# Kernel optimization log

Hardware: AMD Instinct MI355X
Metric: run time of the kernel (lower is better)

Reference implementation:

```python
import jax, jax.numpy as jnp
import numpy as np

N = 50000      # nodes
R = 4          # relations
E = 1600000    # edges per relation
IN = 256       # in_feats
H = 256        # h_feats
C = 16         # num_classes


def setup_inputs() -> dict:
    key = jax.random.key(0)
    ks = jax.random.split(key, 8)
    X = jax.random.normal(ks[0], (N, IN), jnp.float32)
    edge_index = jax.random.randint(ks[1], (R, 2, E), 0, N, dtype=jnp.int32)
    W1 = jax.random.normal(ks[2], (R, IN, H), jnp.float32) * (1.0 / np.sqrt(IN))
    W2 = jax.random.normal(ks[3], (R, H, H), jnp.float32) * (1.0 / np.sqrt(H))
    att_q = jax.random.normal(ks[4], (H,), jnp.float32) * (1.0 / np.sqrt(H))
    tau = jnp.asarray(2.0, jnp.float32)
    W_out = jax.random.normal(ks[5], (H, C), jnp.float32) * (1.0 / np.sqrt(H))
    b_out = jnp.zeros((C,), jnp.float32)
    return {"X": X, "edge_index": edge_index, "W1": W1, "W2": W2,
            "att_q": att_q, "tau": tau, "W_out": W_out, "b_out": b_out}


def _sym_norm_spmm(edge, feat):
    """out = D^{-1/2} A D^{-1/2} @ feat for one relation, edge: [2,E]."""
    row, col = edge[0], edge[1]
    ones = jnp.ones(edge.shape[1], feat.dtype)
    deg_r = jax.ops.segment_sum(ones, row, num_segments=N)
    deg_c = jax.ops.segment_sum(ones, col, num_segments=N)
    dinv_r = jax.lax.rsqrt(jnp.maximum(deg_r, 1.0))
    dinv_c = jax.lax.rsqrt(jnp.maximum(deg_c, 1.0))
    w = dinv_r[row] * dinv_c[col]                      # [E]
    msg = w[:, None] * feat[col]                       # gather + scale
    return jax.ops.segment_sum(msg, row, num_segments=N)  # [N, F]


def _rel_layer(edge_index, feat, W):
    # vmapped over relations: ReLU(A_r feat W_r) -> [R, N, H]
    def one(edge, Wr):
        return jax.nn.relu(_sym_norm_spmm(edge, feat) @ Wr)
    return jax.vmap(one)(edge_index, W)


def reference(X, edge_index, W1, W2, att_q, tau, W_out, b_out):
    # Layer 1: mean over relations (eval mode: no dropout)
    H1 = _rel_layer(edge_index, X, W1)        # [R, N, H]
    h1 = H1.mean(axis=0)                      # [N, H]
    # Layer 2 with relation attention
    H2 = _rel_layer(edge_index, h1, W2)       # [R, N, H]
    scores = jnp.einsum('rnh,h->nr', H2, att_q)
    tau_c = jnp.clip(tau, 0.5, 5.0)
    alpha = jax.nn.softmax(scores / tau_c, axis=1)   # [N, R]
    h2_att = jnp.einsum('nr,rnh->nh', alpha, H2)
    h2 = H2.mean(axis=0) + h2_att             # residual fusion
    logits = h2 @ W_out + b_out               # [N, C]
    return logits, alpha
```

## Files before the change

### kernel.cpp

```cpp
#include <hip/hip_runtime.h>
#include <hip/hip_bf16.h>
#include <stdint.h>

#define NODES 50000
#define RELS  4
#define EDGES 1600000
#define FEAT  256
#define NCLS  16
#define MPAD  50048
#define RPS   50016
#define SCHUNK 1024
#define NSBLK  49
#define NCHUNK 64
#define CHUNKE 25000
#define NB     782

typedef __attribute__((ext_vector_type(8))) short short8;
typedef __attribute__((ext_vector_type(8))) unsigned short u16x8;
typedef __attribute__((ext_vector_type(4))) float f32x4;

static __device__ __forceinline__ float bf2f(unsigned short u) {
    return __uint_as_float(((unsigned int)u) << 16);
}
static __device__ __forceinline__ unsigned short f2bf(float f) {
    unsigned int x = __float_as_uint(f);
    unsigned int r = x + 0x7fffu + ((x >> 16) & 1u);
    return (unsigned short)(r >> 16);
}


__global__ __launch_bounds__(256)
void k_bhist(const int* __restrict__ edges, int arr_off, unsigned* __restrict__ part) {
    int chunk = blockIdx.x, rel = blockIdx.y, t = threadIdx.x;
    const int* arr = edges + (size_t)rel * 2 * EDGES + arr_off + (size_t)chunk * CHUNKE;
    __shared__ unsigned h[NB];
    for (int i = t; i < NB; i += 256) h[i] = 0;
    __syncthreads();
    for (int e = t; e < CHUNKE; e += 256) atomicAdd(&h[((unsigned)arr[e]) >> 6], 1u);
    __syncthreads();
    unsigned* po = part + ((size_t)rel * NCHUNK + chunk) * NB;
    for (int i = t; i < NB; i += 256) po[i] = h[i];
}

__global__ __launch_bounds__(256)
void k_bscan(const unsigned* __restrict__ part, unsigned* __restrict__ off,
             unsigned* __restrict__ bbase) {
    int rel = blockIdx.x, t = threadIdx.x;
    const int BPT = 4;
    int b0 = t * BPT;
    unsigned s = 0;
#pragma unroll
    for (int j = 0; j < BPT; ++j) {
        int b = b0 + j;
        unsigned x = 0;
        if (b < NB)
            for (int c = 0; c < NCHUNK; ++c)
                x += part[((size_t)rel * NCHUNK + c) * NB + b];
        s += x;
    }
    __shared__ unsigned sh[256];
    sh[t] = s;
    __syncthreads();
    for (int o = 1; o < 256; o <<= 1) {
        unsigned u = (t >= o) ? sh[t - o] : 0;
        __syncthreads();
        sh[t] += u;
        __syncthreads();
    }
    unsigned base = sh[t] - s;
#pragma unroll
    for (int j = 0; j < BPT; ++j) {
        int b = b0 + j;
        if (b < NB) {
            bbase[rel * (NB + 1) + b] = base;
            unsigned acc = base;
            for (int c = 0; c < NCHUNK; ++c) {
                size_t o2 = ((size_t)rel * NCHUNK + c) * NB + b;
                off[o2] = acc;
                acc += part[o2];
            }
            base = acc;
        }
    }
    if (t == 255) bbase[rel * (NB + 1) + NB] = sh[255];
}

__global__ __launch_bounds__(256)
void k_scatR(const int* __restrict__ edges, const unsigned* __restrict__ off,
             int2* __restrict__ ebuf) {
    int chunk = blockIdx.x, rel = blockIdx.y, t = threadIdx.x;
    const int* rows = edges + (size_t)rel * 2 * EDGES + (size_t)chunk * CHUNKE;
    const int* cols = rows + EDGES;
    __shared__ unsigned cur[NB];
    const unsigned* po = off + ((size_t)rel * NCHUNK + chunk) * NB;
    for (int i = t; i < NB; i += 256) cur[i] = po[i];
    __syncthreads();
    int2* eb = ebuf + (size_t)rel * EDGES;
    for (int e = t; e < CHUNKE; e += 256) {
        int r = rows[e], c = cols[e];
        unsigned pos = atomicAdd(&cur[((unsigned)r) >> 6], 1u);
        eb[pos] = make_int2(r, c);
    }
}

__global__ __launch_bounds__(256)
void k_scatC(const int* __restrict__ edges, const unsigned* __restrict__ off,
             int* __restrict__ cbuf) {
    int chunk = blockIdx.x, rel = blockIdx.y, t = threadIdx.x;
    const int* cols = edges + (size_t)rel * 2 * EDGES + EDGES + (size_t)chunk * CHUNKE;
    __shared__ unsigned cur[NB];
    const unsigned* po = off + ((size_t)rel * NCHUNK + chunk) * NB;
    for (int i = t; i < NB; i += 256) cur[i] = po[i];
    __syncthreads();
    int* cb = cbuf + (size_t)rel * EDGES;
    for (int e = t; e < CHUNKE; e += 256) {
        int c = cols[e];
        unsigned pos = atomicAdd(&cur[((unsigned)c) >> 6], 1u);
        cb[pos] = c;
    }
}

__global__ __launch_bounds__(256)
void k_countR(const int2* __restrict__ ebuf, const unsigned* __restrict__ bbase,
              int* __restrict__ deg_row) {
    int b = blockIdx.x, rel = blockIdx.y, t = threadIdx.x;
    unsigned s = bbase[rel * (NB + 1) + b], e = bbase[rel * (NB + 1) + b + 1];
    __shared__ unsigned cnt[64];
    if (t < 64) cnt[t] = 0;
    __syncthreads();
    const int2* eb = ebuf + (size_t)rel * EDGES;
    for (unsigned i = s + t; i < e; i += 256) atomicAdd(&cnt[eb[i].x & 63], 1u);
    __syncthreads();
    int base = b * 64;
    if (t < 64 && base + t < NODES) deg_row[(size_t)rel * NODES + base + t] = (int)cnt[t];
}

__global__ __launch_bounds__(256)
void k_countC(const int* __restrict__ cbuf, const unsigned* __restrict__ bbase,
              int* __restrict__ deg_col) {
    int b = blockIdx.x, rel = blockIdx.y, t = threadIdx.x;
    unsigned s = bbase[rel * (NB + 1) + b], e = bbase[rel * (NB + 1) + b + 1];
    __shared__ unsigned cnt[64];
    if (t < 64) cnt[t] = 0;
    __syncthreads();
    const int* cb = cbuf + (size_t)rel * EDGES;
    for (unsigned i = s + t; i < e; i += 256) atomicAdd(&cnt[cb[i] & 63], 1u);
    __syncthreads();
    int base = b * 64;
    if (t < 64 && base + t < NODES) deg_col[(size_t)rel * NODES + base + t] = (int)cnt[t];
}

__global__ void k_dinv(const int* __restrict__ deg_row, const int* __restrict__ deg_col,
                       float* dinv_row, float* dinv_col) {
    int idx = blockIdx.x * blockDim.x + threadIdx.x;
    if (idx >= RELS * NODES) return;
    int dr = deg_row[idx]; if (dr < 1) dr = 1;
    int dc = deg_col[idx]; if (dc < 1) dc = 1;
    dinv_row[idx] = rsqrtf((float)dr);
    dinv_col[idx] = rsqrtf((float)dc);
}

__global__ __launch_bounds__(256)
void k_scanA(const int* __restrict__ deg, int* __restrict__ tmp, int* __restrict__ btot) {
    int r = blockIdx.y, blk = blockIdx.x, t = threadIdx.x;
    int i0 = blk * SCHUNK + t * 4;
    const int* d = deg + (size_t)r * NODES;
    int4 v = make_int4(0, 0, 0, 0);
    if (i0 + 3 < NODES) v = *(const int4*)(d + i0);
    else if (i0 < NODES) {
        v.x = d[i0];
        if (i0 + 1 < NODES) v.y = d[i0 + 1];
        if (i0 + 2 < NODES) v.z = d[i0 + 2];
    }
    int s = v.x + v.y + v.z + v.w;
    __shared__ int sh[256];
    sh[t] = s;
    __syncthreads();
    for (int off = 1; off < 256; off <<= 1) {
        int u = (t >= off) ? sh[t - off] : 0;
        __syncthreads();
        sh[t] += u;
        __syncthreads();
    }
    int excl = sh[t] - s;
    int4 o;
    o.x = excl; o.y = excl + v.x; o.z = o.y + v.y; o.w = o.z + v.z;
    int* tp = tmp + (size_t)r * NODES;
    if (i0 + 3 < NODES) *(int4*)(tp + i0) = o;
    else if (i0 < NODES) {
        tp[i0] = o.x;
        if (i0 + 1 < NODES) tp[i0 + 1] = o.y;
        if (i0 + 2 < NODES) tp[i0 + 2] = o.z;
    }
    if (t == 255) btot[r * 64 + blk] = sh[255];
}

__global__ void k_scanB(int* __restrict__ btot, int* __restrict__ row_ptr) {
    int r = blockIdx.x;
    if (threadIdx.x != 0) return;
    int acc = 0;
    for (int b = 0; b < NSBLK; ++b) {
        int v = btot[r * 64 + b];
        btot[r * 64 + b] = acc;
        acc += v;
    }
    row_ptr[r * RPS + NODES] = acc;
}

__global__ __launch_bounds__(256)
void k_scanC(const int* __restrict__ tmp, const int* __restrict__ btot,
             int* __restrict__ row_ptr) {
    int r = blockIdx.y, blk = blockIdx.x, t = threadIdx.x;
    int i0 = blk * SCHUNK + t * 4;
    int off = btot[r * 64 + blk];
    const int* tp = tmp + (size_t)r * NODES;
    int* rp = row_ptr + (size_t)r * RPS;
    if (i0 + 3 < NODES) {
        int4 v = *(const int4*)(tp + i0);
        rp[i0] = v.x + off; rp[i0 + 1] = v.y + off;
        rp[i0 + 2] = v.z + off; rp[i0 + 3] = v.w + off;
    } else if (i0 < NODES) {
        for (int j = 0; j < 4 && i0 + j < NODES; ++j)
            rp[i0 + j] = tp[i0 + j] + off;
    }
}

__global__ __launch_bounds__(256)
void k_place(const int2* __restrict__ ebuf, const unsigned* __restrict__ bbase,
             const int* __restrict__ row_ptr, int* __restrict__ csr_col) {
    int b = blockIdx.x, rel = blockIdx.y, t = threadIdx.x;
    unsigned s = bbase[rel * (NB + 1) + b], e = bbase[rel * (NB + 1) + b + 1];
    __shared__ int cur[64];
    int base = b * 64;
    const int* rp = row_ptr + (size_t)rel * RPS;
    if (t < 64) cur[t] = (base + t < NODES) ? rp[base + t] : 0;
    __syncthreads();
    const int2* eb = ebuf + (size_t)rel * EDGES;
    int* cc = csr_col + (size_t)rel * EDGES;
    for (unsigned i = s + t; i < e; i += 256) {
        int2 ec = eb[i];
        int pos = atomicAdd(&cur[ec.x - base], 1);
        cc[pos] = ec.y;
    }
}


__global__ void k_f2bf(const float* __restrict__ src, unsigned short* __restrict__ dst, int count) {
    int i = blockIdx.x * blockDim.x + threadIdx.x;
    if (i < count) dst[i] = f2bf(src[i]);
}

__global__ void k_wt(const float* __restrict__ W, unsigned short* __restrict__ Wt) {
    int idx = blockIdx.x * blockDim.x + threadIdx.x;
    if (idx >= RELS * FEAT * FEAT) return;
    int r = idx >> 16;
    int rem = idx & 65535;
    int n = rem >> 8;
    int k = rem & 255;
    Wt[idx] = f2bf(W[(size_t)r * FEAT * FEAT + (size_t)k * FEAT + n]);
}


__global__ __launch_bounds__(256)
void k_spmm(const unsigned short* __restrict__ feat, const int* __restrict__ row_ptr,
            const int* __restrict__ csr_col, const float* __restrict__ dinv_row,
            const float* __restrict__ dinv_col, unsigned short* __restrict__ aggbf, int rel) {
    int wave = (blockIdx.x * blockDim.x + threadIdx.x) >> 6;
    int lane = threadIdx.x & 63;
    if (wave >= NODES) return;
    int row = wave;
    int half = lane >> 5;
    int l32  = lane & 31;
    int start = row_ptr[rel * RPS + row];
    int end   = row_ptr[rel * RPS + row + 1];
    const int* cols = csr_col + (size_t)rel * EDGES;
    const float* dc = dinv_col + rel * NODES;
    const unsigned short* fb = feat + l32 * 8;
    float acc[8] = {0.f, 0.f, 0.f, 0.f, 0.f, 0.f, 0.f, 0.f};
    int j = start + half;
    for (; j + 2 < end; j += 4) {
        int c0 = cols[j];
        int c1 = cols[j + 2];
        float w0 = dc[c0];
        float w1 = dc[c1];
        u16x8 u0 = *(const u16x8*)(fb + (size_t)c0 * FEAT);
        u16x8 u1 = *(const u16x8*)(fb + (size_t)c1 * FEAT);
#pragma unroll
        for (int i = 0; i < 8; ++i) acc[i] += w0 * bf2f(u0[i]);
#pragma unroll
        for (int i = 0; i < 8; ++i) acc[i] += w1 * bf2f(u1[i]);
    }
    if (j < end) {
        int c0 = cols[j];
        float w0 = dc[c0];
        u16x8 u0 = *(const u16x8*)(fb + (size_t)c0 * FEAT);
#pragma unroll
        for (int i = 0; i < 8; ++i) acc[i] += w0 * bf2f(u0[i]);
    }
#pragma unroll
    for (int i = 0; i < 8; ++i) acc[i] += __shfl_down(acc[i], 32, 64);
    if (half == 0) {
        float dr = dinv_row[rel * NODES + row];
        u16x8 o;
#pragma unroll
        for (int i = 0; i < 8; ++i) o[i] = f2bf(acc[i] * dr);
        *(u16x8*)(aggbf + (size_t)row * FEAT + l32 * 8) = o;
    }
}


__global__ __launch_bounds__(256)
void k_gemm1(const unsigned short* __restrict__ Abase, const unsigned short* __restrict__ Wt,
             unsigned short* __restrict__ h1bf) {
    __shared__ __align__(16) unsigned short As[128 * 64];
    __shared__ __align__(16) unsigned short Bs[128 * 64];
    int tid = threadIdx.x;
    int wave = tid >> 6, lane = tid & 63;
    int quad = lane >> 4, l16 = lane & 15;
    int wm = (wave & 1) * 64, wn = (wave >> 1) * 64;
    int row0 = blockIdx.x * 128, n0 = blockIdx.y * 128;

    f32x4 hacc[4][4];
#pragma unroll
    for (int mi = 0; mi < 4; ++mi)
#pragma unroll
        for (int ni = 0; ni < 4; ++ni)
            hacc[mi][ni] = (f32x4){0.f, 0.f, 0.f, 0.f};

    for (int r = 0; r < RELS; ++r) {
        const unsigned short* A  = Abase + (size_t)r * MPAD * FEAT;
        const unsigned short* Bt = Wt + (size_t)r * FEAT * FEAT;
        f32x4 acc[4][4];
#pragma unroll
        for (int mi = 0; mi < 4; ++mi)
#pragma unroll
            for (int ni = 0; ni < 4; ++ni)
                acc[mi][ni] = (f32x4){0.f, 0.f, 0.f, 0.f};

        for (int k0 = 0; k0 < FEAT; k0 += 64) {
#pragma unroll
            for (int issue = 0; issue < 4; ++issue) {
                int flat = issue * 256 + tid;
                int row = flat >> 3;
                int gr = flat & 7;
                int sg = gr ^ (row & 7);
                *(uint4*)&As[flat * 8] = *(const uint4*)(A + (size_t)(row0 + row) * FEAT + k0 + sg * 8);
                *(uint4*)&Bs[flat * 8] = *(const uint4*)(Bt + (size_t)(n0 + row) * FEAT + k0 + sg * 8);
            }
            __syncthreads();
#pragma unroll
            for (int ks = 0; ks < 2; ++ks) {
                int g = ks * 4 + quad;
                short8 af[4], bfr[4];
#pragma unroll
                for (int mi = 0; mi < 4; ++mi) {
                    int m = wm + mi * 16 + l16;
                    af[mi] = *(const short8*)&As[m * 64 + ((g ^ (m & 7)) << 3)];
                }
#pragma unroll
                for (int ni = 0; ni < 4; ++ni) {
                    int n = wn + ni * 16 + l16;
                    bfr[ni] = *(const short8*)&Bs[n * 64 + ((g ^ (n & 7)) << 3)];
                }
#pragma unroll
                for (int mi = 0; mi < 4; ++mi)
#pragma unroll
                    for (int ni = 0; ni < 4; ++ni)
                        acc[mi][ni] = __builtin_amdgcn_mfma_f32_16x16x32_bf16(af[mi], bfr[ni], acc[mi][ni], 0, 0, 0);
            }
            __syncthreads();
        }
#pragma unroll
        for (int mi = 0; mi < 4; ++mi)
#pragma unroll
            for (int ni = 0; ni < 4; ++ni)
#pragma unroll
                for (int i = 0; i < 4; ++i) {
                    float v = acc[mi][ni][i];
                    hacc[mi][ni][i] += 0.25f * (v > 0.f ? v : 0.f);
                }
    }

#pragma unroll
    for (int mi = 0; mi < 4; ++mi)
#pragma unroll
        for (int ni = 0; ni < 4; ++ni) {
            int col = n0 + wn + ni * 16 + l16;
#pragma unroll
            for (int i = 0; i < 4; ++i) {
                int row = row0 + wm + mi * 16 + quad * 4 + i;
                if (row < NODES) h1bf[(size_t)row * FEAT + col] = f2bf(hacc[mi][ni][i]);
            }
        }
}

__global__ __launch_bounds__(256)
void k_gemm2(const unsigned short* __restrict__ A, const unsigned short* __restrict__ Bt,
             unsigned short* __restrict__ H2) {
    __shared__ __align__(16) unsigned short As[128 * 64];
    __shared__ __align__(16) unsigned short Bs[128 * 64];
    int tid = threadIdx.x;
    int wave = tid >> 6, lane = tid & 63;
    int quad = lane >> 4, l16 = lane & 15;
    int wm = (wave & 1) * 64, wn = (wave >> 1) * 64;
    int row0 = blockIdx.x * 128, n0 = blockIdx.y * 128;

    f32x4 acc[4][4];
#pragma unroll
    for (int mi = 0; mi < 4; ++mi)
#pragma unroll
        for (int ni = 0; ni < 4; ++ni)
            acc[mi][ni] = (f32x4){0.f, 0.f, 0.f, 0.f};

    for (int k0 = 0; k0 < FEAT; k0 += 64) {
#pragma unroll
        for (int issue = 0; issue < 4; ++issue) {
            int flat = issue * 256 + tid;
            int row = flat >> 3;
            int gr = flat & 7;
            int sg = gr ^ (row & 7);
            *(uint4*)&As[flat * 8] = *(const uint4*)(A + (size_t)(row0 + row) * FEAT + k0 + sg * 8);
            *(uint4*)&Bs[flat * 8] = *(const uint4*)(Bt + (size_t)(n0 + row) * FEAT + k0 + sg * 8);
        }
        __syncthreads();
#pragma unroll
        for (int ks = 0; ks < 2; ++ks) {
            int g = ks * 4 + quad;
            short8 af[4], bfr[4];
#pragma unroll
            for (int mi = 0; mi < 4; ++mi) {
                int m = wm + mi * 16 + l16;
                af[mi] = *(const short8*)&As[m * 64 + ((g ^ (m & 7)) << 3)];
            }
#pragma unroll
            for (int ni = 0; ni < 4; ++ni) {
                int n = wn + ni * 16 + l16;
                bfr[ni] = *(const short8*)&Bs[n * 64 + ((g ^ (n & 7)) << 3)];
            }
#pragma unroll
            for (int mi = 0; mi < 4; ++mi)
#pragma unroll
                for (int ni = 0; ni < 4; ++ni)
                    acc[mi][ni] = __builtin_amdgcn_mfma_f32_16x16x32_bf16(af[mi], bfr[ni], acc[mi][ni], 0, 0, 0);
        }
        __syncthreads();
    }

#pragma unroll
    for (int mi = 0; mi < 4; ++mi)
#pragma unroll
        for (int ni = 0; ni < 4; ++ni) {
            int col = n0 + wn + ni * 16 + l16;
#pragma unroll
            for (int i = 0; i < 4; ++i) {
                int row = row0 + wm + mi * 16 + quad * 4 + i;
                if (row < NODES) {
                    float v = acc[mi][ni][i];
                    H2[(size_t)row * FEAT + col] = f2bf(v > 0.f ? v : 0.f);
                }
            }
        }
}


__global__ __launch_bounds__(256)
void k_attn_out(const unsigned short* __restrict__ H2bf, const float* __restrict__ att_q,
                const float* __restrict__ tau_p, const float* __restrict__ W_out,
                const float* __restrict__ b_out, float* __restrict__ alpha_out,
                float* __restrict__ logits) {
    __shared__ float red[4][64 * 17];
    int tid = threadIdx.x;
    int wid = tid >> 6;
    int lane = tid & 63;
    int gwave = blockIdx.x * 4 + wid;
    int nwaves = gridDim.x * 4;

    float4 q = *(const float4*)(att_q + lane * 4);
    float tau = fminf(fmaxf(tau_p[0], 0.5f), 5.0f);
    float itau = 1.0f / tau;
    f32x4 Wr[4][4];
#pragma unroll
    for (int j = 0; j < 4; ++j)
#pragma unroll
        for (int c4 = 0; c4 < 4; ++c4) {
            float4 w = *(const float4*)(W_out + (size_t)(lane * 4 + j) * NCLS + c4 * 4);
            Wr[j][c4] = (f32x4){w.x, w.y, w.z, w.w};
        }
    float bc = b_out[lane & 15];
    float* myred = &red[wid][0];
    int cls = lane & 15;
    int rb = (lane >> 4) * 16;

    int n = gwave;
    if (n >= NODES) return;
    ushort4 u[RELS];
#pragma unroll
    for (int r = 0; r < RELS; ++r)
        u[r] = *(const ushort4*)(H2bf + ((size_t)r * NODES + n) * FEAT + lane * 4);

    while (n < NODES) {
        int nn = n + nwaves;
        int nc = (nn < NODES) ? nn : n;
        ushort4 un[RELS];
#pragma unroll
        for (int r = 0; r < RELS; ++r)
            un[r] = *(const ushort4*)(H2bf + ((size_t)r * NODES + nc) * FEAT + lane * 4);

        float h[RELS][4];
#pragma unroll
        for (int r = 0; r < RELS; ++r) {
            h[r][0] = bf2f(u[r].x); h[r][1] = bf2f(u[r].y);
            h[r][2] = bf2f(u[r].z); h[r][3] = bf2f(u[r].w);
        }
        float s[RELS];
#pragma unroll
        for (int r = 0; r < RELS; ++r)
            s[r] = h[r][0] * q.x + h[r][1] * q.y + h[r][2] * q.z + h[r][3] * q.w;
#pragma unroll
        for (int off = 1; off < 64; off <<= 1) {
#pragma unroll
            for (int r = 0; r < RELS; ++r) s[r] += __shfl_xor(s[r], off, 64);
        }
        float m = fmaxf(fmaxf(s[0], s[1]), fmaxf(s[2], s[3]));
        float e[RELS];
        float esum = 0.f;
#pragma unroll
        for (int r = 0; r < RELS; ++r) { e[r] = expf((s[r] - m) * itau); esum += e[r]; }
        float inv = 1.0f / esum;
        float a[RELS];
#pragma unroll
        for (int r = 0; r < RELS; ++r) a[r] = e[r] * inv;
        if (lane == 0)
            *(float4*)(alpha_out + (size_t)n * 4) = make_float4(a[0], a[1], a[2], a[3]);

        float w0 = 0.25f + a[0], w1 = 0.25f + a[1], w2 = 0.25f + a[2], w3 = 0.25f + a[3];
        float h2[4];
#pragma unroll
        for (int j = 0; j < 4; ++j)
            h2[j] = w0 * h[0][j] + w1 * h[1][j] + w2 * h[2][j] + w3 * h[3][j];

        f32x4 acc[4];
#pragma unroll
        for (int c4 = 0; c4 < 4; ++c4)
            acc[c4] = h2[0] * Wr[0][c4] + h2[1] * Wr[1][c4]
                    + h2[2] * Wr[2][c4] + h2[3] * Wr[3][c4];

#pragma unroll
        for (int c4 = 0; c4 < 4; ++c4)
#pragma unroll
            for (int i = 0; i < 4; ++i)
                myred[lane * 17 + c4 * 4 + i] = acc[c4][i];
        asm volatile("s_waitcnt lgkmcnt(0)" ::: "memory");
        float t = 0.f;
#pragma unroll
        for (int k = 0; k < 16; ++k) t += myred[(rb + k) * 17 + cls];
        t += __shfl_xor(t, 16, 64);
        t += __shfl_xor(t, 32, 64);
        if (lane < 16) logits[(size_t)n * NCLS + lane] = t + bc;
        asm volatile("" ::: "memory");

#pragma unroll
        for (int r = 0; r < RELS; ++r) u[r] = un[r];
        n = nn;
    }
}


static inline int cdiv(int a, int b) { return (a + b - 1) / b; }

extern "C" void kernel_launch(void* const* d_in, const int* in_sizes, int n_in,
                              void* d_out, int out_size, void* d_ws, size_t ws_size,
                              hipStream_t stream) {
    const float* X     = (const float*)d_in[0];
    const int*   edges = (const int*)d_in[1];
    const float* W1    = (const float*)d_in[2];
    const float* W2    = (const float*)d_in[3];
    const float* att_q = (const float*)d_in[4];
    const float* tau   = (const float*)d_in[5];
    const float* W_out = (const float*)d_in[6];
    const float* b_out = (const float*)d_in[7];

    float* logits = (float*)d_out;
    float* alpha  = logits + (size_t)NODES * NCLS;

    char* p = (char*)d_ws;
    auto carve = [&](size_t bytes) -> char* {
        char* q = p;
        p += (bytes + 255) & ~(size_t)255;
        return q;
    };
    int*   deg_row  = (int*)carve((size_t)RELS * NODES * 4);
    int*   deg_col  = (int*)carve((size_t)RELS * NODES * 4);
    float* dinv_row = (float*)carve((size_t)RELS * NODES * 4);
    float* dinv_col = (float*)carve((size_t)RELS * NODES * 4);
    int*   row_ptr  = (int*)carve((size_t)RELS * RPS * 4 + 256);
    int*   tmp      = (int*)carve((size_t)RELS * NODES * 4);
    int*   btot     = (int*)carve((size_t)RELS * 64 * 4);
    int*   csr_col  = (int*)carve((size_t)RELS * EDGES * 4);
    unsigned short* Xbf  = (unsigned short*)carve((size_t)NODES * FEAT * 2);
    unsigned short* h1bf = (unsigned short*)carve((size_t)NODES * FEAT * 2);
    unsigned short* W1t  = (unsigned short*)carve((size_t)RELS * FEAT * FEAT * 2);
    unsigned short* W2t  = (unsigned short*)carve((size_t)RELS * FEAT * FEAT * 2);
    const size_t AGGS = (size_t)MPAD * FEAT * 2;
    char* BIG = carve(AGGS + (size_t)RELS * NODES * FEAT * 2);
    int2*     ebuf = (int2*)BIG;
    int*      cbuf = (int*)(BIG + (size_t)RELS * EDGES * 8);
    char*     q = BIG + (size_t)RELS * EDGES * 12;
    unsigned* partR = (unsigned*)q;               q += (size_t)RELS * NCHUNK * NB * 4;
    unsigned* offR  = (unsigned*)q;               q += (size_t)RELS * NCHUNK * NB * 4;
    unsigned* partC = (unsigned*)q;               q += (size_t)RELS * NCHUNK * NB * 4;
    unsigned* offC  = (unsigned*)q;               q += (size_t)RELS * NCHUNK * NB * 4;
    unsigned* bbR   = (unsigned*)q;               q += (size_t)RELS * (NB + 1) * 4;
    unsigned* bbC   = (unsigned*)q;
    unsigned short* aggbf = (unsigned short*)BIG;
    unsigned short* H2bf  = (unsigned short*)(BIG + AGGS);

    {
        dim3 hg(NCHUNK, RELS);
        dim3 bg(NB, RELS);
        k_bhist<<<hg, 256, 0, stream>>>(edges, 0, partR);
        k_bhist<<<hg, 256, 0, stream>>>(edges, EDGES, partC);
        k_bscan<<<RELS, 256, 0, stream>>>(partR, offR, bbR);
        k_bscan<<<RELS, 256, 0, stream>>>(partC, offC, bbC);
        k_scatR<<<hg, 256, 0, stream>>>(edges, offR, ebuf);
        k_scatC<<<hg, 256, 0, stream>>>(edges, offC, cbuf);
        k_countR<<<bg, 256, 0, stream>>>(ebuf, bbR, deg_row);
        k_countC<<<bg, 256, 0, stream>>>(cbuf, bbC, deg_col);
        k_dinv<<<cdiv(RELS * NODES, 256), 256, 0, stream>>>(deg_row, deg_col, dinv_row, dinv_col);
        dim3 sg(NSBLK, RELS);
        k_scanA<<<sg, 256, 0, stream>>>(deg_row, tmp, btot);
        k_scanB<<<RELS, 64, 0, stream>>>(btot, row_ptr);
        k_scanC<<<sg, 256, 0, stream>>>(tmp, btot, row_ptr);
        k_place<<<bg, 256, 0, stream>>>(ebuf, bbR, row_ptr, csr_col);
    }

    k_f2bf<<<cdiv(NODES * FEAT, 256), 256, 0, stream>>>(X, Xbf, NODES * FEAT);
    k_wt<<<cdiv(RELS * FEAT * FEAT, 256), 256, 0, stream>>>(W1, W1t);
    k_wt<<<cdiv(RELS * FEAT * FEAT, 256), 256, 0, stream>>>(W2, W2t);

    dim3 gemm_grid(MPAD / 128, FEAT / 128);

    for (int r = 0; r < RELS; ++r)
        k_spmm<<<cdiv(NODES * 64, 256), 256, 0, stream>>>(Xbf, row_ptr, csr_col,
                                                          dinv_row, dinv_col,
                                                          aggbf + (size_t)r * MPAD * FEAT, r);
    k_gemm1<<<gemm_grid, 256, 0, stream>>>(aggbf, W1t, h1bf);

    for (int r = 0; r < RELS; ++r) {
        k_spmm<<<cdiv(NODES * 64, 256), 256, 0, stream>>>(h1bf, row_ptr, csr_col,
                                                          dinv_row, dinv_col, aggbf, r);
        k_gemm2<<<gemm_grid, 256, 0, stream>>>(aggbf, W2t + (size_t)r * FEAT * FEAT,
                                               H2bf + (size_t)r * NODES * FEAT);
    }

    k_attn_out<<<1024, 256, 0, stream>>>(H2bf, att_q, tau, W_out, b_out, alpha, logits);
}
```

Baseline: 1.523 ms.

## Chunk feature matrix by columns so SpMM gathers hit cache-resident slices

Rearranges the bf16 feature matrix into 8 column chunks of 32 features each, stored contiguously per chunk. The SpMM then runs one chunk at a time per block, with 16 edge groups per wave each loading 64 bytes, and reduces across groups with xor shuffles. Each chunk's feature slice is about 3.2 MB, so random neighbour gathers should stay in L2/LLC instead of thrashing across the full 25 MB matrix. The cost is that column indices and the row pointer are reread once per chunk, a transpose kernel is added, and the edge-index loads and output stores use nontemporal hints.

After: 2.285 ms. 50.0% more time.

```diff
diff --git a/kernel.cpp b/kernel.cpp
--- a/kernel.cpp
+++ b/kernel.cpp
@@ -14,6 +14,8 @@
 #define NCHUNK 64
 #define CHUNKE 25000
 #define NB     782
+#define FCH    8
+#define FCW    32
 
 typedef __attribute__((ext_vector_type(8))) short short8;
 typedef __attribute__((ext_vector_type(8))) unsigned short u16x8;
@@ -260,51 +262,75 @@
     Wt[idx] = f2bf(W[(size_t)r * FEAT * FEAT + (size_t)k * FEAT + n]);
 }
 
-
-__global__ __launch_bounds__(256)
-void k_spmm(const unsigned short* __restrict__ feat, const int* __restrict__ row_ptr,
-            const int* __restrict__ csr_col, const float* __restrict__ dinv_row,
-            const float* __restrict__ dinv_col, unsigned short* __restrict__ aggbf, int rel) {
-    int wave = (blockIdx.x * blockDim.x + threadIdx.x) >> 6;
+__global__ __launch_bounds__(256)
+void k_chunk(const unsigned short* __restrict__ src, unsigned short* __restrict__ dst) {
+    int gid = blockIdx.x * 256 + threadIdx.x;
+    if (gid >= NODES * 32) return;
+    int node = gid >> 5, sub = gid & 31;
+    int chunk = sub >> 2, fl = sub & 3;
+    u16x8 v = *(const u16x8*)(src + (size_t)node * FEAT + sub * 8);
+    *(u16x8*)(dst + ((size_t)chunk * NODES + node) * FCW + fl * 8) = v;
+}
+
+
+__global__ __launch_bounds__(256)
+void k_spmmc(const unsigned short* __restrict__ featc, const int* __restrict__ row_ptr,
+             const int* __restrict__ csr_col, const float* __restrict__ dinv_row,
+             const float* __restrict__ dinv_col, unsigned short* __restrict__ agg,
+             int rel_fixed) {
+    int rel, chunk;
+    unsigned short* aggp;
+    if (rel_fixed < 0) {
+        rel = blockIdx.y; chunk = blockIdx.z;
+        aggp = agg + (size_t)rel * MPAD * FEAT;
+    } else {
+        rel = rel_fixed; chunk = blockIdx.y;
+        aggp = agg;
+    }
+    int wid = threadIdx.x >> 6;
+    int row = blockIdx.x * 4 + wid;
+    if (row >= NODES) return;
     int lane = threadIdx.x & 63;
-    if (wave >= NODES) return;
-    int row = wave;
-    int half = lane >> 5;
-    int l32  = lane & 31;
+    int egrp = lane >> 2, fl = lane & 3;
+
     int start = row_ptr[rel * RPS + row];
     int end   = row_ptr[rel * RPS + row + 1];
     const int* cols = csr_col + (size_t)rel * EDGES;
     const float* dc = dinv_col + rel * NODES;
-    const unsigned short* fb = feat + l32 * 8;
+    const unsigned short* ft = featc + (size_t)chunk * NODES * FCW + fl * 8;
+
     float acc[8] = {0.f, 0.f, 0.f, 0.f, 0.f, 0.f, 0.f, 0.f};
-    int j = start + half;
-    for (; j + 2 < end; j += 4) {
-        int c0 = cols[j];
-        int c1 = cols[j + 2];
+    int j = start + egrp;
+    for (; j + 16 < end; j += 32) {
+        int c0 = __builtin_nontemporal_load(cols + j);
+        int c1 = __builtin_nontemporal_load(cols + j + 16);
         float w0 = dc[c0];
         float w1 = dc[c1];
-        u16x8 u0 = *(const u16x8*)(fb + (size_t)c0 * FEAT);
-        u16x8 u1 = *(const u16x8*)(fb + (size_t)c1 * FEAT);
+        u16x8 u0 = *(const u16x8*)(ft + (size_t)c0 * FCW);
+        u16x8 u1 = *(const u16x8*)(ft + (size_t)c1 * FCW);
 #pragma unroll
         for (int i = 0; i < 8; ++i) acc[i] += w0 * bf2f(u0[i]);
 #pragma unroll
         for (int i = 0; i < 8; ++i) acc[i] += w1 * bf2f(u1[i]);
     }
     if (j < end) {
-        int c0 = cols[j];
+        int c0 = __builtin_nontemporal_load(cols + j);
         float w0 = dc[c0];
-        u16x8 u0 = *(const u16x8*)(fb + (size_t)c0 * FEAT);
+        u16x8 u0 = *(const u16x8*)(ft + (size_t)c0 * FCW);
 #pragma unroll
         for (int i = 0; i < 8; ++i) acc[i] += w0 * bf2f(u0[i]);
     }
 #pragma unroll
-    for (int i = 0; i < 8; ++i) acc[i] += __shfl_down(acc[i], 32, 64);
-    if (half == 0) {
+    for (int off = 4; off < 64; off <<= 1) {
+#pragma unroll
+        for (int i = 0; i < 8; ++i) acc[i] += __shfl_xor(acc[i], off, 64);
+    }
+    if (egrp == 0) {
         float dr = dinv_row[rel * NODES + row];
         u16x8 o;
 #pragma unroll
         for (int i = 0; i < 8; ++i) o[i] = f2bf(acc[i] * dr);
-        *(u16x8*)(aggbf + (size_t)row * FEAT + l32 * 8) = o;
+        __builtin_nontemporal_store(o, (u16x8*)(aggp + (size_t)row * FEAT + chunk * FCW + fl * 8));
     }
 }
 
@@ -614,6 +640,8 @@
     unsigned* bbC   = (unsigned*)q;
     unsigned short* aggbf = (unsigned short*)BIG;
     unsigned short* H2bf  = (unsigned short*)(BIG + AGGS);
+    unsigned short* Xc  = h1bf;
+    unsigned short* h1c = Xbf;
 
     {
         dim3 hg(NCHUNK, RELS);
@@ -640,15 +668,19 @@
 
     dim3 gemm_grid(MPAD / 128, FEAT / 128);
 
-    for (int r = 0; r < RELS; ++r)
-        k_spmm<<<cdiv(NODES * 64, 256), 256, 0, stream>>>(Xbf, row_ptr, csr_col,
-                                                          dinv_row, dinv_col,
-                                                          aggbf + (size_t)r * MPAD * FEAT, r);
+    k_chunk<<<cdiv(NODES * 32, 256), 256, 0, stream>>>(Xbf, Xc);
+    {
+        dim3 sgrid(NODES / 4, RELS, FCH);
+        k_spmmc<<<sgrid, 256, 0, stream>>>(Xc, row_ptr, csr_col, dinv_row, dinv_col,
+                                           aggbf, -1);
+    }
     k_gemm1<<<gemm_grid, 256, 0, stream>>>(aggbf, W1t, h1bf);
 
+    k_chunk<<<cdiv(NODES * 32, 256), 256, 0, stream>>>(h1bf, h1c);
     for (int r = 0; r < RELS; ++r) {
-        k_spmm<<<cdiv(NODES * 64, 256), 256, 0, stream>>>(h1bf, row_ptr, csr_col,
-                                                          dinv_row, dinv_col, aggbf, r);
+        dim3 sgrid(NODES / 4, FCH);
+        k_spmmc<<<sgrid, 256, 0, stream>>>(h1c, row_ptr, csr_col, dinv_row, dinv_col,
+                                           aggbf, r);
         k_gemm2<<<gemm_grid, 256, 0, stream>>>(aggbf, W2t + (size_t)r * FEAT * FEAT,
                                                H2bf + (size_t)r * NODES * FEAT);
     }
```

## Batch per-relation SpMM launches into one grid and vectorize fp32-to-bf16 conversion

Applied to the files above, without the earlier changes.

The four per-relation SpMM launches in each layer become a single launch, with the relation taken from blockIdx.y. This gives more concurrent waves and fewer launches. Layer 2 now aggregates all relations into slices 1..4 of a five-slice buffer. Each GEMM2 then writes its output into the slice just below its input, so H2 overlaps the aggregation buffer in place, and the attention kernel's strides change to MPAD. The X conversion kernel now handles 8 elements per thread with vector loads and stores. The in-place slice aliasing relies on GEMM r finishing before GEMM r+1 overwrites slice r+1, and serialized stream order provides that.

Result: faster. 1.476 ms (-3.1%).

```diff
diff --git a/kernel.cpp b/kernel.cpp
--- a/kernel.cpp
+++ b/kernel.cpp
@@ -245,9 +245,17 @@
 }
 
 
-__global__ void k_f2bf(const float* __restrict__ src, unsigned short* __restrict__ dst, int count) {
-    int i = blockIdx.x * blockDim.x + threadIdx.x;
-    if (i < count) dst[i] = f2bf(src[i]);
+__global__ __launch_bounds__(256)
+void k_f2bf8(const float* __restrict__ src, unsigned short* __restrict__ dst, int count8) {
+    int i = blockIdx.x * 256 + threadIdx.x;
+    if (i >= count8) return;
+    const float* s = src + (size_t)i * 8;
+    float4 a = *(const float4*)s;
+    float4 b = *(const float4*)(s + 4);
+    u16x8 v;
+    v[0] = f2bf(a.x); v[1] = f2bf(a.y); v[2] = f2bf(a.z); v[3] = f2bf(a.w);
+    v[4] = f2bf(b.x); v[5] = f2bf(b.y); v[6] = f2bf(b.z); v[7] = f2bf(b.w);
+    *(u16x8*)(dst + (size_t)i * 8) = v;
 }
 
 __global__ void k_wt(const float* __restrict__ W, unsigned short* __restrict__ Wt) {
@@ -264,7 +272,10 @@
 __global__ __launch_bounds__(256)
 void k_spmm(const unsigned short* __restrict__ feat, const int* __restrict__ row_ptr,
             const int* __restrict__ csr_col, const float* __restrict__ dinv_row,
-            const float* __restrict__ dinv_col, unsigned short* __restrict__ aggbf, int rel) {
+            const float* __restrict__ dinv_col, unsigned short* __restrict__ aggbase,
+            int slice_off) {
+    int rel = blockIdx.y;
+    unsigned short* aggbf = aggbase + (size_t)(rel + slice_off) * (size_t)MPAD * FEAT;
     int wave = (blockIdx.x * blockDim.x + threadIdx.x) >> 6;
     int lane = threadIdx.x & 63;
     if (wave >= NODES) return;
@@ -496,7 +507,7 @@
     ushort4 u[RELS];
 #pragma unroll
     for (int r = 0; r < RELS; ++r)
-        u[r] = *(const ushort4*)(H2bf + ((size_t)r * NODES + n) * FEAT + lane * 4);
+        u[r] = *(const ushort4*)(H2bf + ((size_t)r * MPAD + n) * FEAT + lane * 4);
 
     while (n < NODES) {
         int nn = n + nwaves;
@@ -504,7 +515,7 @@
         ushort4 un[RELS];
 #pragma unroll
         for (int r = 0; r < RELS; ++r)
-            un[r] = *(const ushort4*)(H2bf + ((size_t)r * NODES + nc) * FEAT + lane * 4);
+            un[r] = *(const ushort4*)(H2bf + ((size_t)r * MPAD + nc) * FEAT + lane * 4);
 
         float h[RELS][4];
 #pragma unroll
@@ -601,8 +612,8 @@
     unsigned short* h1bf = (unsigned short*)carve((size_t)NODES * FEAT * 2);
     unsigned short* W1t  = (unsigned short*)carve((size_t)RELS * FEAT * FEAT * 2);
     unsigned short* W2t  = (unsigned short*)carve((size_t)RELS * FEAT * FEAT * 2);
-    const size_t AGGS = (size_t)MPAD * FEAT * 2;
-    char* BIG = carve(AGGS + (size_t)RELS * NODES * FEAT * 2);
+    const size_t AGGSE = (size_t)MPAD * FEAT;
+    char* BIG = carve(5 * AGGSE * 2);
     int2*     ebuf = (int2*)BIG;
     int*      cbuf = (int*)(BIG + (size_t)RELS * EDGES * 8);
     char*     q = BIG + (size_t)RELS * EDGES * 12;
@@ -613,7 +624,7 @@
     unsigned* bbR   = (unsigned*)q;               q += (size_t)RELS * (NB + 1) * 4;
     unsigned* bbC   = (unsigned*)q;
     unsigned short* aggbf = (unsigned short*)BIG;
-    unsigned short* H2bf  = (unsigned short*)(BIG + AGGS);
+    unsigned short* H2bf  = (unsigned short*)BIG;
 
     {
         dim3 hg(NCHUNK, RELS);
@@ -634,24 +645,23 @@
         k_place<<<bg, 256, 0, stream>>>(ebuf, bbR, row_ptr, csr_col);
     }
 
-    k_f2bf<<<cdiv(NODES * FEAT, 256), 256, 0, stream>>>(X, Xbf, NODES * FEAT);
     k_wt<<<cdiv(RELS * FEAT * FEAT, 256), 256, 0, stream>>>(W1, W1t);
     k_wt<<<cdiv(RELS * FEAT * FEAT, 256), 256, 0, stream>>>(W2, W2t);
+    k_f2bf8<<<cdiv(NODES * FEAT / 8, 256), 256, 0, stream>>>(X, Xbf, NODES * FEAT / 8);
 
     dim3 gemm_grid(MPAD / 128, FEAT / 128);
-
+    dim3 spmm_grid(cdiv(NODES * 64, 256), RELS);
+
+    k_spmm<<<spmm_grid, 256, 0, stream>>>(Xbf, row_ptr, csr_col, dinv_row, dinv_col,
+                                          aggbf, 0);
+    k_gemm1<<<gemm_grid, 256, 0, stream>>>(aggbf, W1t, h1bf);
+
+    k_spmm<<<spmm_grid, 256, 0, stream>>>(h1bf, row_ptr, csr_col, dinv_row, dinv_col,
+                                          aggbf, 1);
     for (int r = 0; r < RELS; ++r)
-        k_spmm<<<cdiv(NODES * 64, 256), 256, 0, stream>>>(Xbf, row_ptr, csr_col,
-                                                          dinv_row, dinv_col,
-                                                          aggbf + (size_t)r * MPAD * FEAT, r);
-    k_gemm1<<<gemm_grid, 256, 0, stream>>>(aggbf, W1t, h1bf);
-
-    for (int r = 0; r < RELS; ++r) {
-        k_spmm<<<cdiv(NODES * 64, 256), 256, 0, stream>>>(h1bf, row_ptr, csr_col,
-                                                          dinv_row, dinv_col, aggbf, r);
-        k_gemm2<<<gemm_grid, 256, 0, stream>>>(aggbf, W2t + (size_t)r * FEAT * FEAT,
-                                               H2bf + (size_t)r * NODES * FEAT);
-    }
+        k_gemm2<<<gemm_grid, 256, 0, stream>>>(aggbf + (size_t)(r + 1) * AGGSE,
+                                               W2t + (size_t)r * FEAT * FEAT,
+                                               aggbf + (size_t)r * AGGSE);
 
     k_attn_out<<<1024, 256, 0, stream>>>(H2bf, att_q, tau, W_out, b_out, alpha, logits);
 }
```
